# Kernel optimization log

Measured on AMD Instinct MI355X. Metric: run time of the kernel, lower is better.

## Reference

```python
import jax, jax.numpy as jnp
import numpy as np

EPS = 1e-5
NUM_HEADS = 16
HEAD_DIM = 64


def layernorm(x, g, b):
    mu = jnp.mean(x, axis=-1, keepdims=True)
    var = jnp.mean(jnp.square(x - mu), axis=-1, keepdims=True)
    return (x - mu) * jax.lax.rsqrt(var + EPS) * g + b


def setup_inputs() -> dict:
    key = jax.random.key(0)
    ks = jax.random.split(key, 10)
    B, S, Q, D = 4, 4096, 256, 1024
    x = jax.random.normal(ks[0], (B, S, D), dtype=jnp.float32)
    queries = jax.random.normal(ks[1], (B, Q, D), dtype=jnp.float32)
    attn_mask = jax.random.randint(ks[2], (B, NUM_HEADS, Q, S), 0, 2) == 1
    key_padding_mask = jax.random.randint(ks[3], (B, S), 0, 2) == 1
    scale = 1.0 / np.sqrt(2.0 * D)  # xavier-ish
    Wq = jax.random.normal(ks[4], (D, D), dtype=jnp.float32) * scale
    Wk = jax.random.normal(ks[5], (D, D), dtype=jnp.float32) * scale
    Wv = jax.random.normal(ks[6], (D, D), dtype=jnp.float32) * scale
    Wo = jax.random.normal(ks[7], (D, D), dtype=jnp.float32) * scale
    ln1_g = jnp.ones((D,), jnp.float32); ln1_b = jnp.zeros((D,), jnp.float32)
    ln2_g = jnp.ones((D,), jnp.float32); ln2_b = jnp.zeros((D,), jnp.float32)
    return {"x": x, "queries": queries, "attn_mask": attn_mask,
            "key_padding_mask": key_padding_mask, "Wq": Wq, "Wk": Wk,
            "Wv": Wv, "Wo": Wo, "ln1_g": ln1_g, "ln1_b": ln1_b,
            "ln2_g": ln2_g, "ln2_b": ln2_b}


def reference(x, queries, attn_mask, key_padding_mask, Wq, Wk, Wv, Wo,
              ln1_g, ln1_b, ln2_g, ln2_b):
    B, S, D = x.shape
    Q = queries.shape[1]
    H, hd = NUM_HEADS, HEAD_DIM

    xn = layernorm(x, ln1_g, ln1_b)
    q = (queries @ Wq.T).reshape(B, Q, H, hd)
    k = (xn @ Wk.T).reshape(B, S, H, hd)
    v = (xn @ Wv.T).reshape(B, S, H, hd)

    # scores: (B, H, Q, S)
    scores = jnp.einsum('bqhd,bshd->bhqs', q, k) / np.sqrt(hd)

    mask = attn_mask | key_padding_mask[:, None, None, :]
    neg_inf = jnp.float32(-jnp.inf)
    masked = jnp.where(mask, neg_inf, scores)
    all_masked = jnp.all(mask, axis=-1, keepdims=True)  # rows fully masked
    safe = jnp.where(all_masked, 0.0, masked)
    attn = jax.nn.softmax(safe, axis=-1)
    attn = jnp.where(all_masked, 0.0, attn)

    out = jnp.einsum('bhqs,bshd->bqhd', attn, v).reshape(B, Q, D)
    out = layernorm(out, ln2_g, ln2_b)
    return out @ Wo.T, attn.mean(axis=1)
```

## Files before the change

kernel.cpp:

```cpp
#include <hip/hip_runtime.h>
#include <math.h>

#define DEV __device__ __forceinline__

typedef float  f4v  __attribute__((ext_vector_type(4)));
typedef __bf16 b8v  __attribute__((ext_vector_type(8)));
typedef short  s8v  __attribute__((ext_vector_type(8)));

DEV short f2b(float f){ __bf16 h = (__bf16)f; return __builtin_bit_cast(short, h); }
DEV float b2f(short s){ __bf16 h = __builtin_bit_cast(__bf16, s); return (float)h; }

DEV void gload16(const void* g, void* l){
  __builtin_amdgcn_global_load_lds((const __attribute__((address_space(1))) void*)g,
                                   (__attribute__((address_space(3))) void*)l, 16, 0, 0);
}

DEV b8v ldsf(const short* p){ return __builtin_bit_cast(b8v, *(const s8v*)p); }

DEV f4v mfma16(b8v a, b8v b, f4v c){ return __builtin_amdgcn_mfma_f32_16x16x32_bf16(a, b, c, 0, 0, 0); }

DEV void lds_barrier(){
  asm volatile("s_waitcnt lgkmcnt(0)" ::: "memory");
  __builtin_amdgcn_s_barrier();
}

__global__ __launch_bounds__(256) void prep_kernel(const float* __restrict__ x, const float* __restrict__ ln1g,
                                                   const float* __restrict__ ln1b, short* __restrict__ xn,
                                                   const float* __restrict__ s0, const float* __restrict__ s1,
                                                   const float* __restrict__ s2, const float* __restrict__ s3,
                                                   const float* __restrict__ s4,
                                                   short* __restrict__ d0, short* __restrict__ d1,
                                                   short* __restrict__ d2, short* __restrict__ d3,
                                                   short* __restrict__ d4){
  int bid = blockIdx.x, tid = threadIdx.x;
  if (bid < 5120){
    int i = bid*256 + tid;
    int buf = i >> 18, j = i & 262143;
    const float* s = (buf==0)?s0:(buf==1)?s1:(buf==2)?s2:(buf==3)?s3:s4;
    short*       d = (buf==0)?d0:(buf==1)?d1:(buf==2)?d2:(buf==3)?d3:d4;
    float4 v = ((const float4*)s)[j];
    ((short4*)d)[j] = make_short4(f2b(v.x), f2b(v.y), f2b(v.z), f2b(v.w));
    return;
  }
  int row = bid - 5120;
  const float4 v = ((const float4*)(x + (size_t)row*1024))[tid];
  float s = v.x + v.y + v.z + v.w;
  #pragma unroll
  for (int off=1; off<64; off<<=1) s += __shfl_xor(s, off);
  __shared__ float red[4];
  if ((tid&63)==0) red[tid>>6] = s;
  __syncthreads();
  float mu = (red[0]+red[1]+red[2]+red[3]) * (1.0f/1024.0f);
  float e0=v.x-mu, e1=v.y-mu, e2=v.z-mu, e3=v.w-mu;
  float q = e0*e0 + e1*e1 + e2*e2 + e3*e3;
  #pragma unroll
  for (int off=1; off<64; off<<=1) q += __shfl_xor(q, off);
  __syncthreads();
  if ((tid&63)==0) red[tid>>6] = q;
  __syncthreads();
  float rs = rsqrtf((red[0]+red[1]+red[2]+red[3]) * (1.0f/1024.0f) + 1e-5f);
  float4 g4 = ((const float4*)ln1g)[tid];
  float4 b4 = ((const float4*)ln1b)[tid];
  short4 o = make_short4(f2b(e0*rs*g4.x + b4.x), f2b(e1*rs*g4.y + b4.y),
                         f2b(e2*rs*g4.z + b4.z), f2b(e3*rs*g4.w + b4.w));
  ((short4*)(xn + (size_t)row*1024))[tid] = o;
}

__global__ __launch_bounds__(256) void ln_reduce_kernel(const short* __restrict__ opart, const float* __restrict__ gg,
                                                        const float* __restrict__ bb, short* __restrict__ out){
  int row = blockIdx.x, tid = threadIdx.x;
  float a0=0.f, a1=0.f, a2=0.f, a3=0.f;
  #pragma unroll
  for (int sc=0; sc<32; ++sc){
    short4 t = ((const short4*)(opart + ((size_t)sc*1024 + row)*1024))[tid];
    a0 += b2f(t.x); a1 += b2f(t.y); a2 += b2f(t.z); a3 += b2f(t.w);
  }
  float s = a0 + a1 + a2 + a3;
  #pragma unroll
  for (int off=1; off<64; off<<=1) s += __shfl_xor(s, off);
  __shared__ float red[4];
  if ((tid&63)==0) red[tid>>6] = s;
  __syncthreads();
  float mu = (red[0]+red[1]+red[2]+red[3]) * (1.0f/1024.0f);
  float d0=a0-mu, d1=a1-mu, d2=a2-mu, d3=a3-mu;
  float q = d0*d0 + d1*d1 + d2*d2 + d3*d3;
  #pragma unroll
  for (int off=1; off<64; off<<=1) q += __shfl_xor(q, off);
  __syncthreads();
  if ((tid&63)==0) red[tid>>6] = q;
  __syncthreads();
  float rs = rsqrtf((red[0]+red[1]+red[2]+red[3]) * (1.0f/1024.0f) + 1e-5f);
  float4 g4 = ((const float4*)gg)[tid];
  float4 b4 = ((const float4*)bb)[tid];
  short4 o = make_short4(f2b(d0*rs*g4.x + b4.x), f2b(d1*rs*g4.y + b4.y),
                         f2b(d2*rs*g4.z + b4.z), f2b(d3*rs*g4.w + b4.w));
  ((short4*)(out + (size_t)row*1024))[tid] = o;
}

template<int OUTF32>
__global__ __launch_bounds__(256) void gemm_small(const short* __restrict__ A, const short* __restrict__ B,
                                                  void* __restrict__ C, int M, int N, int K){
  __shared__ short sA[2][64*64];
  __shared__ short sB[2][64*64];
  int tid=threadIdx.x, lane=tid&63, wv=tid>>6, g=lane>>4, r=lane&15;
  int wr=wv>>1, wc=wv&1;
  int m0=blockIdx.x*64, n0=blockIdx.y*64;
  f4v z = {0.f,0.f,0.f,0.f};
  f4v acc[2][2];
  #pragma unroll
  for (int i=0;i<2;++i){
    #pragma unroll
    for (int j=0;j<2;++j) acc[i][j]=z;
  }
  auto stage = [&](int buf, int kt){
    #pragma unroll
    for (int i=0;i<2;++i){
      int idx = i*256 + tid;
      int row = idx>>3, cbs = (idx&7)^(row&7);
      gload16(A + (size_t)(m0+row)*K + kt*64 + cbs*8, &sA[buf][(i*256+wv*64)*8]);
      gload16(B + (size_t)(n0+row)*K + kt*64 + cbs*8, &sB[buf][(i*256+wv*64)*8]);
    }
  };
  int nkt = K >> 6;
  stage(0, 0);
  for (int kt=0; kt<nkt; ++kt){
    int cur = kt & 1;
    if (kt+1 < nkt){
      stage(cur^1, kt+1);
      asm volatile("s_waitcnt vmcnt(4)" ::: "memory");
    } else {
      asm volatile("s_waitcnt vmcnt(0)" ::: "memory");
    }
    __builtin_amdgcn_s_barrier();
    b8v af[2][2], bf[2][2];
    #pragma unroll
    for (int mf=0;mf<2;++mf){
      #pragma unroll
      for (int ks=0;ks<2;++ks){
        int ra = wr*32 + mf*16 + r;
        int rb = wc*32 + mf*16 + r;
        af[mf][ks] = ldsf(&sA[cur][ra*64 + (((ks*4+g)^(ra&7))*8)]);
        bf[mf][ks] = ldsf(&sB[cur][rb*64 + (((ks*4+g)^(rb&7))*8)]);
      }
    }
    #pragma unroll
    for (int mf=0;mf<2;++mf){
      #pragma unroll
      for (int nf=0;nf<2;++nf){
        acc[mf][nf] = mfma16(af[mf][0], bf[nf][0], acc[mf][nf]);
        acc[mf][nf] = mfma16(af[mf][1], bf[nf][1], acc[mf][nf]);
      }
    }
    asm volatile("s_waitcnt lgkmcnt(0)" ::: "memory");
    __builtin_amdgcn_s_barrier();
  }
  #pragma unroll
  for (int mf=0;mf<2;++mf){
    #pragma unroll
    for (int nf=0;nf<2;++nf){
      #pragma unroll
      for (int j=0;j<4;++j){
        int m = m0 + wr*32 + mf*16 + g*4 + j;
        int n = n0 + wc*32 + nf*16 + r;
        if (OUTF32) ((float*)C)[(size_t)m*N + n] = acc[mf][nf][j];
        else        ((short*)C)[(size_t)m*N + n] = f2b(acc[mf][nf][j]);
      }
    }
  }
}

__global__ __launch_bounds__(512,1) void gemm_dual8(const short* __restrict__ A, const short* __restrict__ B0,
                                                    const short* __restrict__ B1, short* __restrict__ C0,
                                                    short* __restrict__ vt){
  __shared__ short sA[2][256*64];
  __shared__ short sBK[2][128*64];
  __shared__ short sBV[2][128*64];
  int tid=threadIdx.x, lane=tid&63, wv=tid>>6, g=lane>>4, r=lane&15;
  int wr=wv>>2, wc=wv&3;
  int m0 = blockIdx.x*256, n0 = blockIdx.y*128;
  f4v z = {0.f,0.f,0.f,0.f};
  f4v ac0[8][2], ac1[8][2];
  #pragma unroll
  for (int i=0;i<8;++i){
    #pragma unroll
    for (int j=0;j<2;++j){ ac0[i][j]=z; ac1[i][j]=z; }
  }
  auto stageA = [&](int buf, int kt, int h){
    #pragma unroll
    for (int ii=0; ii<2; ++ii){
      int idx = ii*512 + tid;
      int rl = idx>>3, cs = (idx&7)^(rl&7);
      int rowA = (((rl>>6)&1)<<7) | (h<<6) | (rl&63);
      gload16(A + (size_t)(m0+rowA)*1024 + kt*64 + cs*8,
              &sA[buf][(h*1024 + ii*512 + wv*64)*8]);
    }
  };
  auto stageBK = [&](int buf, int kt){
    #pragma unroll
    for (int ii=0; ii<2; ++ii){
      int idx = ii*512 + tid;
      int rl = idx>>3, cs = (idx&7)^(rl&7);
      gload16(B0 + (size_t)(n0+rl)*1024 + kt*64 + cs*8, &sBK[buf][(ii*512+wv*64)*8]);
    }
  };
  auto stageBV = [&](int buf, int kt){
    #pragma unroll
    for (int ii=0; ii<2; ++ii){
      int idx = ii*512 + tid;
      int rl = idx>>3, cs = (idx&7)^(rl&7);
      gload16(B1 + (size_t)(n0+rl)*1024 + kt*64 + cs*8, &sBV[buf][(ii*512+wv*64)*8]);
    }
  };
  stageA(0,0,0); stageBK(0,0); stageBV(0,0); stageA(0,0,1);

  b8v af[4][2], bk[2][2], bv[2][2];
  #pragma unroll 2
  for (int t=0; t<16; ++t){
    int cur = t&1, nxt = cur^1;
    asm volatile("s_waitcnt vmcnt(4)" ::: "memory");
    __builtin_amdgcn_s_barrier();
    __builtin_amdgcn_sched_barrier(0);
    if (t < 15) stageA(nxt, t+1, 0);
    #pragma unroll
    for (int ml=0;ml<4;++ml){
      int lr = wr*64 + ml*16 + r;
      #pragma unroll
      for (int ks=0;ks<2;++ks)
        af[ml][ks] = ldsf(&sA[cur][lr*64 + (((ks*4+g)^(r&7))*8)]);
    }
    #pragma unroll
    for (int nf=0;nf<2;++nf){
      int lr = wc*32 + nf*16 + r;
      #pragma unroll
      for (int ks=0;ks<2;++ks)
        bk[nf][ks] = ldsf(&sBK[cur][lr*64 + (((ks*4+g)^(r&7))*8)]);
    }
    __builtin_amdgcn_s_setprio(1);
    #pragma unroll
    for (int ml=0;ml<4;++ml){
      #pragma unroll
      for (int nf=0;nf<2;++nf){
        ac0[ml][nf] = mfma16(af[ml][0], bk[nf][0], ac0[ml][nf]);
        ac0[ml][nf] = mfma16(af[ml][1], bk[nf][1], ac0[ml][nf]);
      }
    }
    __builtin_amdgcn_s_setprio(0);
    if (t < 15) { asm volatile("s_waitcnt vmcnt(4)" ::: "memory"); }
    else        { asm volatile("s_waitcnt vmcnt(2)" ::: "memory"); }
    __builtin_amdgcn_s_barrier();
    __builtin_amdgcn_sched_barrier(0);
    if (t < 15) stageBK(nxt, t+1);
    #pragma unroll
    for (int nf=0;nf<2;++nf){
      int lr = wc*32 + nf*16 + r;
      #pragma unroll
      for (int ks=0;ks<2;++ks)
        bv[nf][ks] = ldsf(&sBV[cur][lr*64 + (((ks*4+g)^(r&7))*8)]);
    }
    __builtin_amdgcn_s_setprio(1);
    #pragma unroll
    for (int ml=0;ml<4;++ml){
      #pragma unroll
      for (int nf=0;nf<2;++nf){
        ac1[ml][nf] = mfma16(af[ml][0], bv[nf][0], ac1[ml][nf]);
        ac1[ml][nf] = mfma16(af[ml][1], bv[nf][1], ac1[ml][nf]);
      }
    }
    __builtin_amdgcn_s_setprio(0);
    if (t < 15) { asm volatile("s_waitcnt vmcnt(4)" ::: "memory"); }
    else        { asm volatile("s_waitcnt vmcnt(0)" ::: "memory"); }
    __builtin_amdgcn_s_barrier();
    __builtin_amdgcn_sched_barrier(0);
    if (t < 15) stageBV(nxt, t+1);
    #pragma unroll
    for (int ml=0;ml<4;++ml){
      int lr = 128 + wr*64 + ml*16 + r;
      #pragma unroll
      for (int ks=0;ks<2;++ks)
        af[ml][ks] = ldsf(&sA[cur][lr*64 + (((ks*4+g)^(r&7))*8)]);
    }
    __builtin_amdgcn_s_setprio(1);
    #pragma unroll
    for (int ml=0;ml<4;++ml){
      #pragma unroll
      for (int nf=0;nf<2;++nf){
        ac0[4+ml][nf] = mfma16(af[ml][0], bk[nf][0], ac0[4+ml][nf]);
        ac0[4+ml][nf] = mfma16(af[ml][1], bk[nf][1], ac0[4+ml][nf]);
      }
    }
    __builtin_amdgcn_s_setprio(0);
    if (t < 15) stageA(nxt, t+1, 1);
    __builtin_amdgcn_s_setprio(1);
    #pragma unroll
    for (int ml=0;ml<4;++ml){
      #pragma unroll
      for (int nf=0;nf<2;++nf){
        ac1[4+ml][nf] = mfma16(af[ml][0], bv[nf][0], ac1[4+ml][nf]);
        ac1[4+ml][nf] = mfma16(af[ml][1], bv[nf][1], ac1[4+ml][nf]);
      }
    }
    __builtin_amdgcn_s_setprio(0);
  }

  int b = m0 >> 12;
  #pragma unroll
  for (int mh=0; mh<2; ++mh){
    #pragma unroll
    for (int ml=0; ml<4; ++ml){
      #pragma unroll
      for (int nf=0; nf<2; ++nf){
        int m = m0 + wr*128 + mh*64 + ml*16 + g*4;
        int n = n0 + wc*32 + nf*16 + r;
        f4v a = ac0[mh*4+ml][nf];
        #pragma unroll
        for (int j=0;j<4;++j)
          C0[(size_t)(m+j)*1024 + n] = f2b(a[j]);
        f4v vvv = ac1[mh*4+ml][nf];
        int h = n >> 6, hd = n & 63;
        short4 vv = make_short4(f2b(vvv[0]), f2b(vvv[1]), f2b(vvv[2]), f2b(vvv[3]));
        *(short4*)&vt[(size_t)((b*16 + h)*64 + hd)*4096 + (m & 4095)] = vv;
      }
    }
  }
}

__global__ __launch_bounds__(256,2) void lsum_kernel(const short* __restrict__ qp, const short* __restrict__ kb,
                                                     const int* __restrict__ am, const int* __restrict__ kpm,
                                                     unsigned* __restrict__ pm, float* __restrict__ lpart){
  int bid = blockIdx.x;
  int sc = bid & 15, bh = bid >> 4;
  int b = bh >> 4, h = bh & 15;
  int s0 = sc*256;
  __shared__ short sQ[256*64];
  __shared__ short sK[256*64];
  __shared__ unsigned sPM[256*8];
  int tid=threadIdx.x, lane=tid&63, wv=tid>>6, g=lane>>4, r=lane&15;

  #pragma unroll
  for (int i=0;i<8;++i){
    int idx = i*256 + wv*64 + lane;
    int row = idx>>3, cbs = (idx&7)^(row&7);
    gload16(qp + (size_t)(b*256 + row)*1024 + h*64 + cbs*8, &sQ[(i*256+wv*64)*8]);
  }
  #pragma unroll
  for (int i=0;i<8;++i){
    int idx = i*256 + wv*64 + lane;
    int row = idx>>3, cbs = (idx&7)^(row&7);
    gload16(kb + (size_t)(b*4096 + s0 + row)*1024 + h*64 + cbs*8, &sK[(i*256+wv*64)*8]);
  }
  int4 kp = *(const int4*)(kpm + (size_t)b*4096 + s0 + lane*4);
  bool k0 = kp.x!=0, k1 = kp.y!=0, k2 = kp.z!=0, k3 = kp.w!=0;
  #pragma unroll 4
  for (int i=0;i<64;++i){
    int row = wv*64 + i;
    const int4 t = *(const int4*)(am + (size_t)(bh*256 + row)*4096 + s0 + lane*4);
    unsigned long long m0 = __ballot(k0 || (t.x!=0));
    unsigned long long m1 = __ballot(k1 || (t.y!=0));
    unsigned long long m2 = __ballot(k2 || (t.z!=0));
    unsigned long long m3 = __ballot(k3 || (t.w!=0));
    if (lane < 8){
      int jj = lane>>1, hh = lane&1;
      unsigned long long bj = (jj==0)?m0:((jj==1)?m1:((jj==2)?m2:m3));
      unsigned w = (unsigned)(bj >> (hh*32));
      sPM[row*8 + lane] = w;
      pm[(size_t)bid*2048 + row*8 + lane] = w;
    }
  }
  __syncthreads();

  b8v a[4][2];
  #pragma unroll
  for (int mf=0;mf<4;++mf){
    #pragma unroll
    for (int ks=0;ks<2;++ks){
      int q = wv*64 + mf*16 + r;
      a[mf][ks] = ldsf(&sQ[q*64 + (((ks*4+g)^(q&7))*8)]);
    }
  }
  unsigned wmr[4][4][2];
  #pragma unroll
  for (int mf=0;mf<4;++mf){
    #pragma unroll
    for (int jq=0;jq<4;++jq){
      int q = wv*64 + mf*16 + g*4 + jq;
      wmr[mf][jq][0] = sPM[q*8 + (r&3)*2 + 0];
      wmr[mf][jq][1] = sPM[q*8 + (r&3)*2 + 1];
    }
  }
  float lacc[4][4];
  #pragma unroll
  for (int mf=0;mf<4;++mf){
    #pragma unroll
    for (int j=0;j<4;++j) lacc[mf][j] = 0.f;
  }
  f4v z = {0.f,0.f,0.f,0.f};
  #pragma unroll 4
  for (int nf=0;nf<16;++nf){
    int srow = nf*16 + r;
    b8v b0 = ldsf(&sK[srow*64 + ((g^(srow&7))*8)]);
    b8v b1 = ldsf(&sK[srow*64 + (((4+g)^(srow&7))*8)]);
    f4v acc[4];
    #pragma unroll
    for (int mf=0;mf<4;++mf){
      acc[mf] = mfma16(a[mf][0], b0, z);
      acc[mf] = mfma16(a[mf][1], b1, acc[mf]);
    }
    int bitp = 4*(nf&7) + (r>>2);
    #pragma unroll
    for (int mf=0;mf<4;++mf){
      #pragma unroll
      for (int j=0;j<4;++j){
        bool mskd = (wmr[mf][j][nf>>3] >> bitp) & 1u;
        lacc[mf][j] += mskd ? 0.f : __expf(acc[mf][j]*0.125f);
      }
    }
  }
  #pragma unroll
  for (int off=1; off<16; off<<=1){
    #pragma unroll
    for (int mf=0;mf<4;++mf){
      #pragma unroll
      for (int j=0;j<4;++j) lacc[mf][j] += __shfl_xor(lacc[mf][j], off);
    }
  }
  if (r == 0){
    #pragma unroll
    for (int mf=0;mf<4;++mf){
      #pragma unroll
      for (int j=0;j<4;++j){
        int q = wv*64 + mf*16 + g*4 + j;
        lpart[(size_t)bid*256 + q] = lacc[mf][j];
      }
    }
  }
}

__global__ void lcomb_kernel(const float* __restrict__ lpart, float* __restrict__ linv){
  int row = blockIdx.x*256 + threadIdx.x;
  int q = row & 255, bh = row >> 8;
  float l = 0.f;
  #pragma unroll
  for (int sc=0; sc<16; ++sc) l += lpart[(size_t)(bh*16+sc)*256 + q];
  linv[row] = (l > 0.f) ? (1.0f/l) : 0.f;
}

__global__ __launch_bounds__(512,4) void attn_pv_kernel(const short* __restrict__ qp, const short* __restrict__ kb,
                                                        const short* __restrict__ vt, const unsigned* __restrict__ pm,
                                                        const float* __restrict__ linv, short* __restrict__ opart,
                                                        float* __restrict__ out2){
  int bid = blockIdx.x;
  int sc = bid & 31, qt = (bid>>5)&3, b = bid>>7;
  int s0 = sc*128, q0 = qt*64;
  int half = sc & 1, scq = sc >> 1;
  __shared__ short sK[128*64];
  __shared__ short sV[64*128];
  __shared__ short sQ[64*64];
  __shared__ unsigned sPM[64*4];
  int tid=threadIdx.x, lane=tid&63, wv=tid>>6, g=lane>>4, r=lane&15;
  int wq = wv>>2, ws = wv&3;
  f4v z = {0.f,0.f,0.f,0.f};
  float macc[2][2][4];
  #pragma unroll
  for (int sb=0;sb<2;++sb){
    #pragma unroll
    for (int qb=0;qb<2;++qb){
      #pragma unroll
      for (int j=0;j<4;++j) macc[sb][qb][j] = 0.f;
    }
  }

  for (int h=0; h<16; ++h){
    int bh = b*16 + h;
    { int row = tid>>3, cbs = (tid&7)^(row&7);
      gload16(qp + (size_t)(b*256 + q0 + row)*1024 + h*64 + cbs*8, &sQ[(wv*64)*8]); }
    #pragma unroll
    for (int i=0;i<2;++i){
      int idx = i*512 + tid;
      int row = idx>>3, cbs = (idx&7)^(row&7);
      gload16(kb + (size_t)(b*4096 + s0 + row)*1024 + h*64 + cbs*8, &sK[(i*512+wv*64)*8]);
    }
    #pragma unroll
    for (int i=0;i<2;++i){
      int idx = i*512 + tid;
      int row = idx>>4, sl = idx&15, sls = sl^(row&7);
      gload16(vt + (size_t)(bh*64 + row)*4096 + s0 + sls*8, &sV[(i*512+wv*64)*8]);
    }
    if (tid < 256)
      sPM[tid] = pm[(size_t)(bh*16+scq)*2048 + (q0 + (tid>>2))*8 + (tid&3)*2 + half];
    __syncthreads();

    b8v qf[2][2];
    #pragma unroll
    for (int qb=0;qb<2;++qb){
      #pragma unroll
      for (int ks=0;ks<2;++ks){
        int qrow = wq*32 + qb*16 + r;
        qf[qb][ks] = ldsf(&sQ[qrow*64 + (((ks*4+g)^(qrow&7))*8)]);
      }
    }
    f4v accs[2][2];
    __builtin_amdgcn_s_setprio(1);
    #pragma unroll
    for (int sb=0;sb<2;++sb){
      int srow = ws*32 + sb*16 + r;
      b8v k0 = ldsf(&sK[srow*64 + ((g^(srow&7))*8)]);
      b8v k1 = ldsf(&sK[srow*64 + (((4+g)^(srow&7))*8)]);
      #pragma unroll
      for (int qb=0;qb<2;++qb){
        accs[sb][qb] = mfma16(k0, qf[qb][0], z);
        accs[sb][qb] = mfma16(k1, qf[qb][1], accs[sb][qb]);
      }
    }
    __builtin_amdgcn_s_setprio(0);
    lds_barrier();

    float iv[2];
    iv[0] = linv[(size_t)bh*256 + q0 + wq*32 + r];
    iv[1] = linv[(size_t)bh*256 + q0 + wq*32 + 16 + r];
    unsigned wmq[2][4];
    #pragma unroll
    for (int qb=0;qb<2;++qb){
      #pragma unroll
      for (int j=0;j<4;++j)
        wmq[qb][j] = sPM[(wq*32+qb*16+r)*4 + j];
    }
    short* P = &sK[0];
    #pragma unroll
    for (int sb=0;sb<2;++sb){
      int bitp = ws*8 + sb*4 + g;
      #pragma unroll
      for (int qb=0;qb<2;++qb){
        float pj[4];
        #pragma unroll
        for (int j=0;j<4;++j){
          bool mskd = (wmq[qb][j] >> bitp) & 1u;
          pj[j] = mskd ? 0.f : __expf(accs[sb][qb][j]*0.125f) * iv[qb];
          macc[sb][qb][j] += pj[j];
        }
        int q = wq*32 + qb*16 + r;
        unsigned lo = ((unsigned)(unsigned short)f2b(pj[0])) | (((unsigned)(unsigned short)f2b(pj[1]))<<16);
        unsigned hi = ((unsigned)(unsigned short)f2b(pj[2])) | (((unsigned)(unsigned short)f2b(pj[3]))<<16);
        int sbase = (ws*32 + sb*16 + g*4) ^ ((q&7)<<3);
        uint2 pk; pk.x = lo; pk.y = hi;
        *(uint2*)&P[q*128 + sbase] = pk;
      }
    }
    lds_barrier();

    f4v acco[2]; acco[0]=z; acco[1]=z;
    __builtin_amdgcn_s_setprio(1);
    #pragma unroll
    for (int ks=0;ks<4;++ks){
      int vrow = ws*16 + r;
      b8v bv = ldsf(&sV[vrow*128 + ((ks*32+g*8) ^ ((vrow&7)<<3))]);
      #pragma unroll
      for (int mf=0;mf<2;++mf){
        int prow = wq*32 + mf*16 + r;
        b8v ap = ldsf(&P[prow*128 + ((ks*32+g*8) ^ ((prow&7)<<3))]);
        acco[mf] = mfma16(ap, bv, acco[mf]);
      }
    }
    __builtin_amdgcn_s_setprio(0);
    #pragma unroll
    for (int mf=0;mf<2;++mf){
      #pragma unroll
      for (int j=0;j<4;++j)
        opart[((size_t)sc*1024 + b*256 + q0 + wq*32 + mf*16 + g*4 + j)*1024 + h*64 + ws*16 + r] = f2b(acco[mf][j]);
    }
    lds_barrier();
  }

  #pragma unroll
  for (int sb=0;sb<2;++sb){
    #pragma unroll
    for (int qb=0;qb<2;++qb){
      int q = q0 + wq*32 + qb*16 + r;
      float4 o = make_float4(macc[sb][qb][0]*0.0625f, macc[sb][qb][1]*0.0625f,
                             macc[sb][qb][2]*0.0625f, macc[sb][qb][3]*0.0625f);
      *(float4*)&out2[(size_t)(b*256 + q)*4096 + s0 + ws*32 + sb*16 + g*4] = o;
    }
  }
}

extern "C" void kernel_launch(void* const* d_in, const int* in_sizes, int n_in,
                              void* d_out, int out_size, void* d_ws, size_t ws_size,
                              hipStream_t stream){
  const float* x       = (const float*)d_in[0];
  const float* queries = (const float*)d_in[1];
  const int*   am      = (const int*)d_in[2];
  const int*   kpm     = (const int*)d_in[3];
  const float* Wq      = (const float*)d_in[4];
  const float* Wk      = (const float*)d_in[5];
  const float* Wv      = (const float*)d_in[6];
  const float* Wo      = (const float*)d_in[7];
  const float* ln1g    = (const float*)d_in[8];
  const float* ln1b    = (const float*)d_in[9];
  const float* ln2g    = (const float*)d_in[10];
  const float* ln2b    = (const float*)d_in[11];
  float* out0 = (float*)d_out;
  float* out2 = out0 + (size_t)4*256*1024;
  char* ws = (char*)d_ws;

  size_t off = 0;
  auto alloc = [&](size_t bytes){ void* p = ws + off; off += (bytes + 255) & ~(size_t)255; return p; };
  short*    xn   = (short*)alloc(33554432);
  short*    kb   = (short*)alloc(33554432);
  short*    vt   = (short*)alloc(33554432);
  short*    wqb  = (short*)alloc(2097152);
  short*    wkb  = (short*)alloc(2097152);
  short*    wvb  = (short*)alloc(2097152);
  short*    wob  = (short*)alloc(2097152);
  short*    qbf  = (short*)alloc(2097152);
  short*    qpj  = (short*)alloc(2097152);
  unsigned* pmw  = (unsigned*)alloc(8388608);
  float*    lpart= (float*)alloc(1048576);
  float*    linv = (float*)alloc(65536);
  short*    opart= (short*)alloc(67108864);
  short*    onb  = (short*)alloc(2097152);

  prep_kernel<<<21504,256,0,stream>>>(x, ln1g, ln1b, xn,
                                      queries, Wq, Wk, Wv, Wo, qbf, wqb, wkb, wvb, wob);
  gemm_dual8<<<dim3(64,8),512,0,stream>>>(xn, wkb, wvb, kb, vt);
  gemm_small<0><<<dim3(16,16),256,0,stream>>>(qbf, wqb, qpj, 1024, 1024, 1024);
  lsum_kernel<<<1024,256,0,stream>>>(qpj, kb, am, kpm, pmw, lpart);
  lcomb_kernel<<<64,256,0,stream>>>(lpart, linv);
  attn_pv_kernel<<<512,512,0,stream>>>(qpj, kb, vt, pmw, linv, opart, out2);
  ln_reduce_kernel<<<1024,256,0,stream>>>(opart, ln2g, ln2b, onb);
  gemm_small<1><<<dim3(16,16),256,0,stream>>>(onb, wob, out0, 1024, 1024, 1024);
}
```

Before: 316.9 us.

## Double-buffer K/V tiles in attn_pv and load Q fragments straight to registers

```diff
diff --git a/kernel.cpp b/kernel.cpp
--- a/kernel.cpp
+++ b/kernel.cpp
@@ -16,6 +16,7 @@
 }
 
 DEV b8v ldsf(const short* p){ return __builtin_bit_cast(b8v, *(const s8v*)p); }
+DEV b8v gldf(const short* p){ return __builtin_bit_cast(b8v, *(const s8v*)p); }
 
 DEV f4v mfma16(b8v a, b8v b, f4v c){ return __builtin_amdgcn_mfma_f32_16x16x32_bf16(a, b, c, 0, 0, 0); }
 
@@ -452,10 +453,9 @@
   int sc = bid & 31, qt = (bid>>5)&3, b = bid>>7;
   int s0 = sc*128, q0 = qt*64;
   int half = sc & 1, scq = sc >> 1;
-  __shared__ short sK[128*64];
-  __shared__ short sV[64*128];
-  __shared__ short sQ[64*64];
-  __shared__ unsigned sPM[64*4];
+  __shared__ short sK[2][128*64];
+  __shared__ short sV[2][64*128];
+  __shared__ unsigned sPM[2][64*4];
   int tid=threadIdx.x, lane=tid&63, wv=tid>>6, g=lane>>4, r=lane&15;
   int wq = wv>>2, ws = wv&3;
   f4v z = {0.f,0.f,0.f,0.f};
@@ -469,62 +469,80 @@
     }
   }
 
-  for (int h=0; h<16; ++h){
+  auto stageKV = [&](int buf, int h){
     int bh = b*16 + h;
-    { int row = tid>>3, cbs = (tid&7)^(row&7);
-      gload16(qp + (size_t)(b*256 + q0 + row)*1024 + h*64 + cbs*8, &sQ[(wv*64)*8]); }
     #pragma unroll
     for (int i=0;i<2;++i){
       int idx = i*512 + tid;
       int row = idx>>3, cbs = (idx&7)^(row&7);
-      gload16(kb + (size_t)(b*4096 + s0 + row)*1024 + h*64 + cbs*8, &sK[(i*512+wv*64)*8]);
+      gload16(kb + (size_t)(b*4096 + s0 + row)*1024 + h*64 + cbs*8, &sK[buf][(i*512+wv*64)*8]);
     }
     #pragma unroll
     for (int i=0;i<2;++i){
       int idx = i*512 + tid;
       int row = idx>>4, sl = idx&15, sls = sl^(row&7);
-      gload16(vt + (size_t)(bh*64 + row)*4096 + s0 + sls*8, &sV[(i*512+wv*64)*8]);
-    }
-    if (tid < 256)
-      sPM[tid] = pm[(size_t)(bh*16+scq)*2048 + (q0 + (tid>>2))*8 + (tid&3)*2 + half];
-    __syncthreads();
-
-    b8v qf[2][2];
-    #pragma unroll
-    for (int qb=0;qb<2;++qb){
-      #pragma unroll
-      for (int ks=0;ks<2;++ks){
-        int qrow = wq*32 + qb*16 + r;
-        qf[qb][ks] = ldsf(&sQ[qrow*64 + (((ks*4+g)^(qrow&7))*8)]);
-      }
-    }
+      gload16(vt + (size_t)(bh*64 + row)*4096 + s0 + sls*8, &sV[buf][(i*512+wv*64)*8]);
+    }
+  };
+  auto pmld = [&](int h)->unsigned {
+    int t = tid & 255;
+    return pm[(size_t)((b*16+h)*16+scq)*2048 + (q0 + (t>>2))*8 + (t&3)*2 + half];
+  };
+
+  stageKV(0, 0);
+  unsigned pmv = pmld(0);
+  b8v qf00 = gldf(qp + (size_t)(b*256 + q0 + wq*32 + r)*1024 + 0*64 + (0*4+g)*8);
+  b8v qf01 = gldf(qp + (size_t)(b*256 + q0 + wq*32 + r)*1024 + 0*64 + (1*4+g)*8);
+  b8v qf10 = gldf(qp + (size_t)(b*256 + q0 + wq*32 + 16 + r)*1024 + 0*64 + (0*4+g)*8);
+  b8v qf11 = gldf(qp + (size_t)(b*256 + q0 + wq*32 + 16 + r)*1024 + 0*64 + (1*4+g)*8);
+  float iv0 = linv[(size_t)(b*16)*256 + q0 + wq*32 + r];
+  float iv1 = linv[(size_t)(b*16)*256 + q0 + wq*32 + 16 + r];
+
+  #pragma unroll 2
+  for (int h=0; h<16; ++h){
+    int cur = h&1, nxt = cur^1;
+    asm volatile("s_waitcnt vmcnt(0)" ::: "memory");
+    if (tid < 256) sPM[cur][tid] = pmv;
+    asm volatile("s_waitcnt lgkmcnt(0)" ::: "memory");
+    __builtin_amdgcn_s_barrier();
+    __builtin_amdgcn_sched_barrier(0);
+
+    b8v qn00, qn01, qn10, qn11; unsigned pmvn = 0; float ivn0 = 0.f, ivn1 = 0.f;
+    if (h < 15){
+      stageKV(nxt, h+1);
+      pmvn = pmld(h+1);
+      size_t qb0 = (size_t)(b*256 + q0 + wq*32 + r)*1024 + (h+1)*64;
+      size_t qb1 = (size_t)(b*256 + q0 + wq*32 + 16 + r)*1024 + (h+1)*64;
+      qn00 = gldf(qp + qb0 + g*8);       qn01 = gldf(qp + qb0 + (4+g)*8);
+      qn10 = gldf(qp + qb1 + g*8);       qn11 = gldf(qp + qb1 + (4+g)*8);
+      ivn0 = linv[(size_t)(b*16+h+1)*256 + q0 + wq*32 + r];
+      ivn1 = linv[(size_t)(b*16+h+1)*256 + q0 + wq*32 + 16 + r];
+    }
+
     f4v accs[2][2];
     __builtin_amdgcn_s_setprio(1);
     #pragma unroll
     for (int sb=0;sb<2;++sb){
       int srow = ws*32 + sb*16 + r;
-      b8v k0 = ldsf(&sK[srow*64 + ((g^(srow&7))*8)]);
-      b8v k1 = ldsf(&sK[srow*64 + (((4+g)^(srow&7))*8)]);
-      #pragma unroll
-      for (int qb=0;qb<2;++qb){
-        accs[sb][qb] = mfma16(k0, qf[qb][0], z);
-        accs[sb][qb] = mfma16(k1, qf[qb][1], accs[sb][qb]);
-      }
+      b8v k0 = ldsf(&sK[cur][srow*64 + ((g^(srow&7))*8)]);
+      b8v k1 = ldsf(&sK[cur][srow*64 + (((4+g)^(srow&7))*8)]);
+      accs[sb][0] = mfma16(k0, qf00, z);
+      accs[sb][0] = mfma16(k1, qf01, accs[sb][0]);
+      accs[sb][1] = mfma16(k0, qf10, z);
+      accs[sb][1] = mfma16(k1, qf11, accs[sb][1]);
     }
     __builtin_amdgcn_s_setprio(0);
     lds_barrier();
 
-    float iv[2];
-    iv[0] = linv[(size_t)bh*256 + q0 + wq*32 + r];
-    iv[1] = linv[(size_t)bh*256 + q0 + wq*32 + 16 + r];
+    float iv[2]; iv[0] = iv0; iv[1] = iv1;
     unsigned wmq[2][4];
     #pragma unroll
     for (int qb=0;qb<2;++qb){
       #pragma unroll
       for (int j=0;j<4;++j)
-        wmq[qb][j] = sPM[(wq*32+qb*16+r)*4 + j];
-    }
-    short* P = &sK[0];
+        wmq[qb][j] = sPM[cur][(wq*32+qb*16+r)*4 + j];
+    }
+    short* P = &sK[cur][0];
     #pragma unroll
     for (int sb=0;sb<2;++sb){
       int bitp = ws*8 + sb*4 + g;
@@ -552,7 +570,7 @@
     #pragma unroll
     for (int ks=0;ks<4;++ks){
       int vrow = ws*16 + r;
-      b8v bv = ldsf(&sV[vrow*128 + ((ks*32+g*8) ^ ((vrow&7)<<3))]);
+      b8v bv = ldsf(&sV[cur][vrow*128 + ((ks*32+g*8) ^ ((vrow&7)<<3))]);
       #pragma unroll
       for (int mf=0;mf<2;++mf){
         int prow = wq*32 + mf*16 + r;
@@ -567,7 +585,9 @@
       for (int j=0;j<4;++j)
         opart[((size_t)sc*1024 + b*256 + q0 + wq*32 + mf*16 + g*4 + j)*1024 + h*64 + ws*16 + r] = f2b(acco[mf][j]);
     }
-    lds_barrier();
+
+    qf00 = qn00; qf01 = qn01; qf10 = qn10; qf11 = qn11;
+    pmv = pmvn; iv0 = ivn0; iv1 = ivn1;
   }
 
   #pragma unroll
```

Result: slower. 377.9 us (+19.3%).
